# Kernel optimization log

Hardware: AMD Instinct MI355X
Metric: run time of the kernel (lower is better)

The kernel has to match this reference:

```python
import jax, jax.numpy as jnp
import numpy as np

V, F, KIN, KSEL, VSEL = 200000, 128, 64, 16, 50000


def setup_inputs() -> dict:
    key = jax.random.key(0)
    k1, k2, k3, k4 = jax.random.split(key, 4)
    features = jax.random.normal(k1, (V, F), dtype=jnp.float32)
    distances = jax.random.uniform(k2, (V, KIN), dtype=jnp.float32)
    # -1 encodes 'missing neighbour' (as in HGCalML kNN convention); allow some -1s
    nidx = jax.random.randint(k3, (V, KIN), -1, V).astype(jnp.int32)
    # first neighbour is the vertex itself, at distance 0 (kNN convention)
    nidx = nidx.at[:, 0].set(jnp.arange(V, dtype=jnp.int32))
    distances = distances.at[:, 0].set(0.0)
    # cluster-centre selection indices (stand-in for LocalCluster custom-op output)
    sel_idx = jax.random.randint(k4, (VSEL, 1), 0, V).astype(jnp.int32)
    return {"features": features, "distances": distances, "nidx": nidx,
            "sel_idx": sel_idx, "K": KSEL}


def reference(features, distances, nidx, sel_idx, K):
    # --- SortAndSelectNeighbours.raw_call (radius < 0 => no radius cut) ---
    BIG = jnp.float32(1e9)
    tfdist = jnp.where(nidx < 0, BIG, distances)          # push missing to the end
    order = jnp.argsort(tfdist, axis=1)                   # [V, KIN]
    snidx = jnp.take_along_axis(nidx, order, axis=1)[:, :K]  # [V, K] int32

    # --- SelectFromIndices: apply cluster-centre selection ---
    sel_nidx = snidx[sel_idx[:, 0]]                       # [VSEL, K]

    # --- GraphClusterReshape.raw_call: gather, zero-pad mask, flatten ---
    safe_idx = jnp.where(sel_nidx < 0, 0, sel_nidx)       # -1 -> 0 for gather
    gfeat = features[safe_idx]                            # [VSEL, K, F]
    gfeat = jnp.where(sel_nidx[..., None] < 0, jnp.float32(0.0), gfeat)
    return gfeat.reshape(sel_idx.shape[0], K * features.shape[1])  # [VSEL, K*F]
```

## Files before the change

kernel.cpp:

```cpp
#include <hip/hip_runtime.h>
#include <stdint.h>

constexpr int F    = 128;
constexpr int KIN  = 64;
constexpr int KSEL = 16;
constexpr int VSEL = 50000;

typedef float f32x4 __attribute__((ext_vector_type(4)));

__global__ __launch_bounds__(256) void lcr_kernel(
    const float* __restrict__ features,
    const float* __restrict__ distances,
    const int*   __restrict__ nidx,
    const int*   __restrict__ sel_idx,
    float*       __restrict__ out)
{
    const int lane = threadIdx.x & 63;
    const int wave = threadIdx.x >> 6;
    const int row  = blockIdx.x * 4 + wave;
    if (row >= VSEL) return;

    const int v = sel_idx[row];

    const float d  = distances[(size_t)v * KIN + lane];
    const int   ni = nidx     [(size_t)v * KIN + lane];

    const uint32_t bits = __float_as_uint(ni < 0 ? 1.0e9f : d);
    uint64_t key = ((uint64_t)bits << 6) | (uint32_t)lane;

    #pragma unroll
    for (int k = 2; k <= 64; k <<= 1) {
        #pragma unroll
        for (int j = k >> 1; j >= 1; j >>= 1) {
            const uint64_t other = __shfl_xor(key, j, 64);
            const bool lower    = (lane & j) == 0;
            const bool asc      = (lane & k) == 0;
            const bool take_min = (lower == asc);
            const bool swap     = take_min ? (other < key) : (other > key);
            key = swap ? other : key;
        }
    }

    const int col       = (int)(key & 63);
    const int sorted_ni = __shfl(ni, col, 64);

    const int half = lane >> 5;
    const int l32  = lane & 31;

    int idxs[8];
    #pragma unroll
    for (int p = 0; p < 8; ++p)
        idxs[p] = __shfl(sorted_ni, 2 * p + half, 64);

    f32x4 vals[8];
    #pragma unroll
    for (int p = 0; p < 8; ++p) {
        const int safe = idxs[p] < 0 ? 0 : idxs[p];
        vals[p] = *reinterpret_cast<const f32x4*>(
                      &features[(size_t)safe * F + l32 * 4]);
    }

    const size_t out_base = (size_t)row * (KSEL * F);
    #pragma unroll
    for (int p = 0; p < 8; ++p) {
        f32x4 val = vals[p];
        if (idxs[p] < 0) { val = (f32x4)(0.0f); }
        __builtin_nontemporal_store(val,
            reinterpret_cast<f32x4*>(&out[out_base + (size_t)(2 * p + half) * F + l32 * 4]));
    }
}

extern "C" void kernel_launch(void* const* d_in, const int* in_sizes, int n_in,
                              void* d_out, int out_size, void* d_ws, size_t ws_size,
                              hipStream_t stream)
{
    const float* features  = (const float*)d_in[0];
    const float* distances = (const float*)d_in[1];
    const int*   nidx      = (const int*)  d_in[2];
    const int*   sel_idx   = (const int*)  d_in[3];
    float* out = (float*)d_out;

    const int rows_per_block = 4;
    const int grid = (VSEL + rows_per_block - 1) / rows_per_block;
    lcr_kernel<<<grid, 256, 0, stream>>>(features, distances, nidx, sel_idx, out);
}
```

Before: 127.2 us.

## Invert gather into per-source scatter using atomic slot map

Instead of each output row gathering 16 feature rows, the launch builds an inverse map: per source vertex it records which output positions need its features, using atomic counters and a fixed-capacity slot array in the workspace. A scatter kernel then reads each source feature row once and writes it to all its destinations, while zero and overflow entries are handled directly in the map-building pass. This is meant to cut redundant random feature reads. In exchange it adds two extra kernel launches, atomics and workspace traffic, and it falls back to the old gather when the workspace is too small.

```diff
diff --git a/kernel.cpp b/kernel.cpp
--- a/kernel.cpp
+++ b/kernel.cpp
@@ -1,14 +1,115 @@
 #include <hip/hip_runtime.h>
 #include <stdint.h>
 
+constexpr int V    = 200000;
 constexpr int F    = 128;
 constexpr int KIN  = 64;
 constexpr int KSEL = 16;
 constexpr int VSEL = 50000;
+constexpr int CAP  = 40;
 
+typedef float f32x2 __attribute__((ext_vector_type(2)));
 typedef float f32x4 __attribute__((ext_vector_type(4)));
 
-__global__ __launch_bounds__(256) void lcr_kernel(
+__global__ __launch_bounds__(256) void zero_counts_kernel(uint32_t* __restrict__ counts)
+{
+    const int i = blockIdx.x * 256 + threadIdx.x;
+    if (i < V) counts[i] = 0;
+}
+
+__global__ __launch_bounds__(256) void build_map_kernel(
+    const float* __restrict__ distances,
+    const int*   __restrict__ nidx,
+    const int*   __restrict__ sel_idx,
+    const float* __restrict__ features,
+    float*       __restrict__ out,
+    uint32_t*    __restrict__ counts,
+    uint32_t*    __restrict__ slots)
+{
+    const int lane = threadIdx.x & 63;
+    const int wave = threadIdx.x >> 6;
+    const int row  = blockIdx.x * 4 + wave;
+    if (row >= VSEL) return;
+
+    const int v = sel_idx[row];
+    const float d  = distances[(size_t)v * KIN + lane];
+    const int   ni = nidx     [(size_t)v * KIN + lane];
+
+    const uint32_t bits = __float_as_uint(ni < 0 ? 1.0e9f : d);
+    uint64_t key = ((uint64_t)bits << 6) | (uint32_t)lane;
+
+    #pragma unroll
+    for (int k = 2; k <= 64; k <<= 1) {
+        #pragma unroll
+        for (int j = k >> 1; j >= 1; j >>= 1) {
+            const uint64_t other = __shfl_xor(key, j, 64);
+            const bool lower    = (lane & j) == 0;
+            const bool asc      = (lane & k) == 0;
+            const bool take_min = (lower == asc);
+            const bool swap     = take_min ? (other < key) : (other > key);
+            key = swap ? other : key;
+        }
+    }
+
+    const int col       = (int)(key & 63);
+    const int sorted_ni = __shfl(ni, col, 64);
+
+    bool ovf = false;
+    if (lane < KSEL && sorted_ni >= 0) {
+        const uint32_t slot = atomicAdd(&counts[sorted_ni], 1u);
+        if (slot < CAP)
+            slots[(size_t)sorted_ni * CAP + slot] = (uint32_t)(row * KSEL + lane);
+        else
+            ovf = true;
+    }
+
+    const uint64_t zmask = __ballot(lane < KSEL && sorted_ni < 0);
+    const uint64_t omask = __ballot(ovf);
+    if (zmask | omask) {
+        const size_t out_base = (size_t)row * (KSEL * F);
+        for (int k = 0; k < KSEL; ++k) {
+            const int  idx = __shfl(sorted_ni, k, 64);
+            const bool isz = (zmask >> k) & 1ull;
+            const bool iso = (omask >> k) & 1ull;
+            if (isz) {
+                f32x2 z = {0.0f, 0.0f};
+                *reinterpret_cast<f32x2*>(&out[out_base + (size_t)k * F + lane * 2]) = z;
+            } else if (iso) {
+                const f32x2 val = *reinterpret_cast<const f32x2*>(
+                                      &features[(size_t)idx * F + lane * 2]);
+                *reinterpret_cast<f32x2*>(&out[out_base + (size_t)k * F + lane * 2]) = val;
+            }
+        }
+    }
+}
+
+__global__ __launch_bounds__(256) void scatter_kernel(
+    const float*    __restrict__ features,
+    const uint32_t* __restrict__ counts,
+    const uint32_t* __restrict__ slots,
+    float*          __restrict__ out)
+{
+    const int lane = threadIdx.x & 63;
+    const int wave = threadIdx.x >> 6;
+    const int v    = blockIdx.x * 4 + wave;
+    if (v >= V) return;
+
+    uint32_t c = counts[v];
+    if (c == 0) return;
+    c = min(c, (uint32_t)CAP);
+
+    uint32_t mypos = 0;
+    if (lane < (int)c) mypos = slots[(size_t)v * CAP + lane];
+
+    const f32x2 val = *reinterpret_cast<const f32x2*>(&features[(size_t)v * F + lane * 2]);
+
+    for (uint32_t j = 0; j < c; ++j) {
+        const uint32_t pos = __shfl(mypos, (int)j, 64);
+        *reinterpret_cast<f32x2*>(&out[(size_t)pos * F + lane * 2]) = val;
+    }
+}
+
+__global__ __launch_bounds__(256) void lcr_gather_kernel(
     const float* __restrict__ features,
     const float* __restrict__ distances,
     const int*   __restrict__ nidx,
@@ -21,10 +122,8 @@
     if (row >= VSEL) return;
 
     const int v = sel_idx[row];
-
     const float d  = distances[(size_t)v * KIN + lane];
     const int   ni = nidx     [(size_t)v * KIN + lane];
-
     const uint32_t bits = __float_as_uint(ni < 0 ? 1.0e9f : d);
     uint64_t key = ((uint64_t)bits << 6) | (uint32_t)lane;
 
@@ -56,15 +155,14 @@
     #pragma unroll
     for (int p = 0; p < 8; ++p) {
         const int safe = idxs[p] < 0 ? 0 : idxs[p];
-        vals[p] = *reinterpret_cast<const f32x4*>(
-                      &features[(size_t)safe * F + l32 * 4]);
+        vals[p] = *reinterpret_cast<const f32x4*>(&features[(size_t)safe * F + l32 * 4]);
     }
 
     const size_t out_base = (size_t)row * (KSEL * F);
     #pragma unroll
     for (int p = 0; p < 8; ++p) {
         f32x4 val = vals[p];
-        if (idxs[p] < 0) { val = (f32x4)(0.0f); }
+        if (idxs[p] < 0) val = (f32x4)(0.0f);
         __builtin_nontemporal_store(val,
             reinterpret_cast<f32x4*>(&out[out_base + (size_t)(2 * p + half) * F + l32 * 4]));
     }
@@ -80,7 +178,17 @@
     const int*   sel_idx   = (const int*)  d_in[3];
     float* out = (float*)d_out;
 
-    const int rows_per_block = 4;
-    const int grid = (VSEL + rows_per_block - 1) / rows_per_block;
-    lcr_kernel<<<grid, 256, 0, stream>>>(features, distances, nidx, sel_idx, out);
+    const size_t need = (size_t)V * (1 + CAP) * sizeof(uint32_t);
+    if (ws_size >= need) {
+        uint32_t* counts = (uint32_t*)d_ws;
+        uint32_t* slots  = counts + V;
+
+        zero_counts_kernel<<<(V + 255) / 256, 256, 0, stream>>>(counts);
+        build_map_kernel<<<(VSEL + 3) / 4, 256, 0, stream>>>(
+            distances, nidx, sel_idx, features, out, counts, slots);
+        scatter_kernel<<<(V + 3) / 4, 256, 0, stream>>>(features, counts, slots, out);
+    } else {
+        lcr_gather_kernel<<<(VSEL + 3) / 4, 256, 0, stream>>>(
+            features, distances, nidx, sel_idx, out);
+    }
 }
```

New measurement: 185.7 us. 46.0% more time.
